# Performance work log

Measured on AMD Instinct MI355X. Metric: run time of the kernel, lower is better.

Reference implementation:

```python
import jax, jax.numpy as jnp
import numpy as np


def setup_inputs() -> dict:
    key = jax.random.key(0)
    ks = jax.random.split(key, 9)
    bs, nf, h, w = 4, 512, 64, 64
    c8 = nf // 8
    sc = 1.0 / np.sqrt(nf)
    return {
        "x": jax.random.normal(ks[0], (bs, nf, h, w), dtype=jnp.float32),
        "Wq": jax.random.normal(ks[1], (c8, nf), dtype=jnp.float32) * sc,
        "bq": jax.random.normal(ks[2], (c8,), dtype=jnp.float32) * 0.01,
        "Wk": jax.random.normal(ks[3], (c8, nf), dtype=jnp.float32) * sc,
        "bk": jax.random.normal(ks[4], (c8,), dtype=jnp.float32) * 0.01,
        "Wv": jax.random.normal(ks[5], (nf, nf), dtype=jnp.float32) * sc,
        "bv": jax.random.normal(ks[6], (nf,), dtype=jnp.float32) * 0.01,
        "alpha": jax.random.normal(ks[7], (1,), dtype=jnp.float32) * 0.1,
    }


def reference(x, Wq, bq, Wk, bk, Wv, bv, alpha):
    bs, nf, h, w = x.shape
    hw = h * w
    xf = x.reshape(bs, nf, hw)  # flatten spatial; 1x1 conv == channel matmul
    q = jnp.einsum('oc,bcn->bon', Wq, xf) + bq[:, None]  # (bs, c8, hw)
    k = jnp.einsum('oc,bcn->bon', Wk, xf) + bk[:, None]  # (bs, c8, hw)
    v = jnp.einsum('oc,bcn->bon', Wv, xf) + bv[:, None]  # (bs, nf, hw)
    # scores[b, i, j] = key_i . query_j ; softmax over j (queries)
    scores = jnp.einsum('bci,bcj->bij', k, q)  # (bs, hw, hw)
    attn = jax.nn.softmax(scores, axis=-1)
    # out[b, c, i] = sum_j v[b, c, j] * attn[b, i, j]
    out = jnp.einsum('bcj,bij->bci', v, attn).reshape(bs, nf, h, w)
    return x + alpha * out
```

## Files before the change

kernel.cpp:

```cpp
#include <hip/hip_runtime.h>

#define BS 4
#define NF 512
#define HW 4096
#define C8 64
#define TI 64
#define JC 64

typedef unsigned short bfu;
typedef __attribute__((ext_vector_type(8))) short bf16x8;
typedef __attribute__((ext_vector_type(4))) float f32x4;

static __device__ __forceinline__ bfu f2bu(float v) {
    union { unsigned int u; float f; } c; c.f = v;
    unsigned int u = c.u;
    u = u + 0x7FFFu + ((u >> 16) & 1u);
    return (bfu)(u >> 16);
}

static __device__ __forceinline__ unsigned int cvt_pk_bf16(float lo, float hi) {
    unsigned int r;
    asm("v_cvt_pk_bf16_f32 %0, %1, %2" : "=v"(r) : "v"(lo), "v"(hi));
    return r;
}

static __device__ __forceinline__ void gload16(const void* g, void* l) {
    __builtin_amdgcn_global_load_lds(
        (const __attribute__((address_space(1))) unsigned int*)g,
        (__attribute__((address_space(3))) unsigned int*)l,
        16, 0, 0);
}

__global__ __launch_bounds__(256) void k0_pre(const float* __restrict__ x, bfu* __restrict__ xt,
                                              const float* __restrict__ Wq, const float* __restrict__ bq,
                                              const float* __restrict__ Wk, const float* __restrict__ bk,
                                              const float* __restrict__ Wv, const float* __restrict__ bv,
                                              bfu* __restrict__ Wb, float* __restrict__ bcat)
{
    __shared__ float T[64][68];
    const int t   = threadIdx.x;
    const int bid = blockIdx.x;

    if (bid >= 2048) {
        const int o = bid - 2048;
        const float* src; float bias;
        if (o < 64)       { src = Wq + (size_t)o * NF;          bias = bq[o]; }
        else if (o < 128) { src = Wk + (size_t)(o - 64) * NF;   bias = bk[o - 64]; }
        else              { src = Wv + (size_t)(o - 128) * NF;  bias = bv[o - 128]; }
        float2 v = *(const float2*)(src + t * 2);
        Wb[(size_t)o * NF + t * 2 + 0] = f2bu(v.x);
        Wb[(size_t)o * NF + t * 2 + 1] = f2bu(v.y);
        if (t == 0) bcat[o] = bias;
        return;
    }

    const int n0 = (bid & 63) * 64;
    const int c0 = ((bid >> 6) & 7) * 64;
    const int b  = bid >> 9;

    #pragma unroll
    for (int u = 0; u < 4; u++) {
        int f4 = u * 256 + t;
        int cc = f4 >> 4;
        int n4 = (f4 & 15) << 2;
        float4 v = *(const float4*)(x + ((size_t)(b * NF + c0 + cc)) * HW + n0 + n4);
        *(float4*)&T[cc][n4 ^ (((cc >> 3) & 3) << 2)] = v;
    }
    __syncthreads();
    #pragma unroll
    for (int u = 0; u < 2; u++) {
        int e8 = u * 256 + t;
        int nn = e8 >> 3;
        int c8 = (e8 & 7) << 3;
        union { int4 i4; bfu h[8]; } pk;
        #pragma unroll
        for (int q = 0; q < 8; q++)
            pk.h[q] = f2bu(T[c8 + q][nn ^ ((((c8 + q) >> 3) & 3) << 2)]);
        *(int4*)(xt + ((size_t)(b * HW + n0 + nn)) * NF + c0 + c8) = pk.i4;
    }
}

__global__ __launch_bounds__(256) void k1_proj(const bfu* __restrict__ Wb, const float* __restrict__ bcat,
                                               const bfu* __restrict__ xt,
                                               bfu* __restrict__ Qb, bfu* __restrict__ Kb, bfu* __restrict__ Vb)
{
    __shared__ bfu As[2][128 * 64];
    __shared__ bfu Bs[2][128 * 64];
    const int t  = threadIdx.x;
    const int o0 = blockIdx.x * 128;
    const int n0 = blockIdx.y * 128;
    const int b  = blockIdx.z;
    const int lane = t & 63, wv = t >> 6;
    const int wm = wv & 1, wn = wv >> 1;
    const int l15 = lane & 15, quad = lane >> 4;
    const int r7  = l15 & 7;
    const int sl0 = (quad ^ r7) * 8;
    const int sl1 = ((quad + 4) ^ r7) * 8;

    const int srow = t >> 3;
    const int scolz = ((t & 7) ^ (srow & 7)) * 8;

    const bfu* gA = Wb + ((size_t)(o0 + srow)) * NF + scolz;
    const bfu* gB = xt + ((size_t)(b * HW + n0 + srow)) * NF + scolz;

    f32x4 acc[4][4];
    #pragma unroll
    for (int m = 0; m < 4; m++)
        #pragma unroll
        for (int n = 0; n < 4; n++) acc[m][n] = (f32x4){0.f, 0.f, 0.f, 0.f};

#define K1_STAGE(buf, c0)                                                       \
    _Pragma("unroll")                                                           \
    for (int p = 0; p < 4; p++) {                                               \
        gload16(gA + (size_t)(p * 32) * NF + (c0), &As[buf][t * 8 + p * 2048]); \
        gload16(gB + (size_t)(p * 32) * NF + (c0), &Bs[buf][t * 8 + p * 2048]); \
    }

#define K1_COMPUTE(pc)                                                                      \
    {                                                                                       \
        bf16x8 Af0[4], Af1[4], Bf0[4], Bf1[4];                                              \
        _Pragma("unroll")                                                                   \
        for (int m = 0; m < 4; m++) {                                                       \
            const bfu* ar = &As[pc][(wm * 64 + m * 16 + l15) * 64];                         \
            Af0[m] = *(const bf16x8*)(ar + sl0);                                            \
            Af1[m] = *(const bf16x8*)(ar + sl1);                                            \
        }                                                                                   \
        _Pragma("unroll")                                                                   \
        for (int n = 0; n < 4; n++) {                                                       \
            const bfu* br = &Bs[pc][(wn * 64 + n * 16 + l15) * 64];                         \
            Bf0[n] = *(const bf16x8*)(br + sl0);                                            \
            Bf1[n] = *(const bf16x8*)(br + sl1);                                            \
        }                                                                                   \
        __builtin_amdgcn_s_setprio(1);                                                      \
        _Pragma("unroll")                                                                   \
        for (int m = 0; m < 4; m++)                                                         \
            _Pragma("unroll")                                                               \
            for (int n = 0; n < 4; n++) {                                                   \
                acc[m][n] = __builtin_amdgcn_mfma_f32_16x16x32_bf16(Af0[m], Bf0[n], acc[m][n], 0, 0, 0); \
                acc[m][n] = __builtin_amdgcn_mfma_f32_16x16x32_bf16(Af1[m], Bf1[n], acc[m][n], 0, 0, 0); \
            }                                                                               \
        __builtin_amdgcn_s_setprio(0);                                                      \
    }

    K1_STAGE(0, 0)
    for (int it = 0; it < 7; it++) {
        const int pc = it & 1;
        K1_STAGE(pc ^ 1, (it + 1) * 64)
        asm volatile("s_waitcnt vmcnt(8)" ::: "memory");
        __builtin_amdgcn_sched_barrier(0);
        __builtin_amdgcn_s_barrier();
        K1_COMPUTE(pc)
        __builtin_amdgcn_sched_barrier(0);
        __builtin_amdgcn_s_barrier();
    }
    asm volatile("s_waitcnt vmcnt(0)" ::: "memory");
    __builtin_amdgcn_sched_barrier(0);
    __builtin_amdgcn_s_barrier();
    K1_COMPUTE(1)
#undef K1_STAGE
#undef K1_COMPUTE

    if (o0 == 0) {
        #pragma unroll
        for (int mt = 0; mt < 4; mt++)
            #pragma unroll
            for (int nt = 0; nt < 4; nt++) {
                int goq = wm * 64 + mt * 16 + quad * 4;
                int n   = n0 + wn * 64 + nt * 16 + l15;
                float v0 = acc[mt][nt][0] + bcat[goq + 0];
                float v1 = acc[mt][nt][1] + bcat[goq + 1];
                float v2 = acc[mt][nt][2] + bcat[goq + 2];
                float v3 = acc[mt][nt][3] + bcat[goq + 3];
                int2 pk;
                pk.x = (int)cvt_pk_bf16(v0, v1);
                pk.y = (int)cvt_pk_bf16(v2, v3);
                if (wm == 0) *(int2*)(Qb + ((size_t)(b * HW + n)) * C8 + goq)      = pk;
                else         *(int2*)(Kb + ((size_t)(b * HW + n)) * C8 + goq - 64) = pk;
            }
    } else {
        #pragma unroll
        for (int mt = 0; mt < 4; mt++)
            #pragma unroll
            for (int nt = 0; nt < 4; nt++)
                #pragma unroll
                for (int r = 0; r < 4; r++) {
                    int go = o0 + wm * 64 + mt * 16 + quad * 4 + r;
                    int n  = n0 + wn * 64 + nt * 16 + l15;
                    float val = acc[mt][nt][r] + bcat[go];
                    Vb[((size_t)(b * NF + (go - 128))) * HW + n] = f2bu(val);
                }
    }
}

__global__ __launch_bounds__(512, 4) void k23_fused(const bfu* __restrict__ Kb, const bfu* __restrict__ Qb,
                                                    const bfu* __restrict__ Vb,
                                                    const float* __restrict__ x, const float* __restrict__ alpha,
                                                    float* __restrict__ out)
{
    __shared__ bfu   Vs[2][256 * 64];
    __shared__ bfu   Ps[64 * 64];
    __shared__ float LSum[8][2][16];
    __shared__ float Scale[TI];

    const int t = threadIdx.x;
    const int lane = t & 63, w = t >> 6;
    const int l15 = lane & 15, quad = lane >> 4;
    const int jq  = w & 3;
    const int iqb = (w >> 2) * 32;

    const int d    = blockIdx.x;
    const int xcd  = d & 7;
    const int b    = xcd >> 1;
    const int cblk = xcd & 1;
    const int i0   = (d >> 3) * TI;

    const bfu* kp0 = Kb + ((size_t)(b * HW + i0 + iqb + l15)) * C8 + quad * 8;
    const bfu* kp1 = kp0 + (size_t)16 * C8;
    const bf16x8 Kf00 = *(const bf16x8*)kp0;
    const bf16x8 Kf01 = *(const bf16x8*)(kp0 + 32);
    const bf16x8 Kf10 = *(const bf16x8*)kp1;
    const bf16x8 Kf11 = *(const bf16x8*)(kp1 + 32);

    const int srow = t >> 3, sslot = t & 7;
    const bfu* gV = Vb + ((size_t)(b * NF + cblk * 256 + srow)) * HW + ((sslot ^ (srow & 7)) * 8);

    const bfu* qbase = Qb + ((size_t)(b * HW + jq * 16 + l15)) * C8 + quad * 8;

    const int r7  = l15 & 7;
    const int sl0 = (quad ^ r7) * 8;
    const int sl1 = ((quad + 4) ^ r7) * 8;
    const int pwz = ((jq * 2 + (quad >> 1)) ^ r7) * 8 + (quad & 1) * 4;

    f32x4 acc[2][4];
    #pragma unroll
    for (int mt = 0; mt < 2; mt++)
        #pragma unroll
        for (int nt = 0; nt < 4; nt++) acc[mt][nt] = (f32x4){0.f, 0.f, 0.f, 0.f};
    float rs0 = 0.f, rs1 = 0.f;
    bf16x8 Aq[2][2];

    Aq[0][0] = *(const bf16x8*)qbase;
    Aq[0][1] = *(const bf16x8*)(qbase + 32);
    #pragma unroll
    for (int p = 0; p < 4; p++)
        gload16(gV + (size_t)(p * 64) * HW, &Vs[0][t * 8 + p * 4096]);
    {
        f32x4 s0 = (f32x4){0.f,0.f,0.f,0.f}, s1 = (f32x4){0.f,0.f,0.f,0.f};
        s0 = __builtin_amdgcn_mfma_f32_16x16x32_bf16(Aq[0][0], Kf00, s0, 0, 0, 0);
        s0 = __builtin_amdgcn_mfma_f32_16x16x32_bf16(Aq[0][1], Kf01, s0, 0, 0, 0);
        s1 = __builtin_amdgcn_mfma_f32_16x16x32_bf16(Aq[0][0], Kf10, s1, 0, 0, 0);
        s1 = __builtin_amdgcn_mfma_f32_16x16x32_bf16(Aq[0][1], Kf11, s1, 0, 0, 0);
        float e0 = __expf(s0[0]), e1 = __expf(s0[1]), e2 = __expf(s0[2]), e3 = __expf(s0[3]);
        float f0 = __expf(s1[0]), f1 = __expf(s1[1]), f2 = __expf(s1[2]), f3 = __expf(s1[3]);
        rs0 += (e0 + e1) + (e2 + e3);
        rs1 += (f0 + f1) + (f2 + f3);
        uint2 pk0, pk1;
        pk0.x = cvt_pk_bf16(e0, e1);  pk0.y = cvt_pk_bf16(e2, e3);
        pk1.x = cvt_pk_bf16(f0, f1);  pk1.y = cvt_pk_bf16(f2, f3);
        *(uint2*)(Ps + (iqb + l15)      * 64 + pwz) = pk0;
        *(uint2*)(Ps + (iqb + 16 + l15) * 64 + pwz) = pk1;
    }

#define K23_ITER(q, pc, pn)                                                                    \
  {                                                                                            \
    const int jn = (((q) + 1) & 63) * JC;                                                      \
                                      \
    {                                                                                          \
        const bfu* qpn = qbase + (size_t)jn * C8;                                              \
        Aq[pn][0] = *(const bf16x8*)qpn;                                                       \
        Aq[pn][1] = *(const bf16x8*)(qpn + 32);                                                \
    }                                                                                          \
    _Pragma("unroll")                                                                          \
    for (int p = 0; p < 4; p++)                                                                \
        gload16(gV + (size_t)(p * 64) * HW + jn, &Vs[pn][t * 8 + p * 4096]);                   \
             \
    asm volatile("s_waitcnt vmcnt(6) lgkmcnt(0)" ::: "memory");                                \
    __builtin_amdgcn_sched_barrier(0);                                                         \
    __builtin_amdgcn_s_barrier();                        \
                    \
    f32x4 s0 = (f32x4){0.f,0.f,0.f,0.f}, s1 = (f32x4){0.f,0.f,0.f,0.f};                        \
    if (jn) {                                                                                  \
        s0 = __builtin_amdgcn_mfma_f32_16x16x32_bf16(Aq[pn][0], Kf00, s0, 0, 0, 0);            \
        s0 = __builtin_amdgcn_mfma_f32_16x16x32_bf16(Aq[pn][1], Kf01, s0, 0, 0, 0);            \
        s1 = __builtin_amdgcn_mfma_f32_16x16x32_bf16(Aq[pn][0], Kf10, s1, 0, 0, 0);            \
        s1 = __builtin_amdgcn_mfma_f32_16x16x32_bf16(Aq[pn][1], Kf11, s1, 0, 0, 0);            \
    }                                                                                          \
                                     \
    {                                                                                          \
        bf16x8 V0[2], V1[2];                                                                   \
        _Pragma("unroll")                                                                      \
        for (int mt = 0; mt < 2; mt++) {                                                       \
            const bfu* vrow = &Vs[pc][(w * 32 + mt * 16 + l15) * 64];                          \
            V0[mt] = *(const bf16x8*)(vrow + sl0);                                             \
            V1[mt] = *(const bf16x8*)(vrow + sl1);                                             \
        }                                                                                      \
        __builtin_amdgcn_s_setprio(1);                                                         \
        _Pragma("unroll")                                                                      \
        for (int nt = 0; nt < 4; nt++) {                                                       \
            const bfu* prow = Ps + (nt * 16 + l15) * 64;                                       \
            bf16x8 Pf0 = *(const bf16x8*)(prow + sl0);                                         \
            bf16x8 Pf1 = *(const bf16x8*)(prow + sl1);                                         \
            _Pragma("unroll")                                                                  \
            for (int mt = 0; mt < 2; mt++) {                                                   \
                acc[mt][nt] = __builtin_amdgcn_mfma_f32_16x16x32_bf16(V0[mt], Pf0, acc[mt][nt], 0, 0, 0); \
                acc[mt][nt] = __builtin_amdgcn_mfma_f32_16x16x32_bf16(V1[mt], Pf1, acc[mt][nt], 0, 0, 0); \
            }                                                                                  \
        }                                                                                      \
        __builtin_amdgcn_s_setprio(0);                                                         \
    }                                                                                          \
    asm volatile("s_waitcnt lgkmcnt(0)" ::: "memory");                                         \
    __builtin_amdgcn_sched_barrier(0);                                                         \
    __builtin_amdgcn_s_barrier();        \
                                 \
    if (jn) {                                                                                  \
        float e0 = __expf(s0[0]), e1 = __expf(s0[1]), e2 = __expf(s0[2]), e3 = __expf(s0[3]);  \
        float f0 = __expf(s1[0]), f1 = __expf(s1[1]), f2 = __expf(s1[2]), f3 = __expf(s1[3]);  \
        rs0 += (e0 + e1) + (e2 + e3);                                                          \
        rs1 += (f0 + f1) + (f2 + f3);                                                          \
        uint2 pk0, pk1;                                                                        \
        pk0.x = cvt_pk_bf16(e0, e1);  pk0.y = cvt_pk_bf16(e2, e3);                             \
        pk1.x = cvt_pk_bf16(f0, f1);  pk1.y = cvt_pk_bf16(f2, f3);                             \
        *(uint2*)(Ps + (iqb + l15)      * 64 + pwz) = pk0;                                     \
        *(uint2*)(Ps + (iqb + 16 + l15) * 64 + pwz) = pk1;                                     \
    }                                                                                          \
  }

    for (int qq = 0; qq < 32; qq++) {
        K23_ITER(2 * qq,     0, 1)
        K23_ITER(2 * qq + 1, 1, 0)
    }
#undef K23_ITER

    float sred0 = rs0, sred1 = rs1;
    sred0 += __shfl_xor(sred0, 16, 64);
    sred0 += __shfl_xor(sred0, 32, 64);
    sred1 += __shfl_xor(sred1, 16, 64);
    sred1 += __shfl_xor(sred1, 32, 64);
    if (quad == 0) { LSum[w][0][l15] = sred0; LSum[w][1][l15] = sred1; }
    __syncthreads();
    if (t < TI) {
        int u = t >> 5, s = (t >> 4) & 1, il = t & 15;
        float L = (LSum[u * 4 + 0][s][il] + LSum[u * 4 + 1][s][il])
                + (LSum[u * 4 + 2][s][il] + LSum[u * 4 + 3][s][il]);
        Scale[t] = alpha[0] / L;
    }
    __syncthreads();

    #pragma unroll
    for (int nt = 0; nt < 4; nt++) {
        float sc = Scale[nt * 16 + l15];
        int i = i0 + nt * 16 + l15;
        #pragma unroll
        for (int mt = 0; mt < 2; mt++)
            #pragma unroll
            for (int r = 0; r < 4; r++) {
                int c = cblk * 256 + w * 32 + mt * 16 + quad * 4 + r;
                size_t idx = ((size_t)(b * NF + c)) * HW + i;
                out[idx] = x[idx] + sc * acc[mt][nt][r];
            }
    }
}

extern "C" void kernel_launch(void* const* d_in, const int* in_sizes, int n_in,
                              void* d_out, int out_size, void* d_ws, size_t ws_size,
                              hipStream_t stream)
{
    const float* x     = (const float*)d_in[0];
    const float* Wq    = (const float*)d_in[1];
    const float* bq    = (const float*)d_in[2];
    const float* Wk    = (const float*)d_in[3];
    const float* bk    = (const float*)d_in[4];
    const float* Wv    = (const float*)d_in[5];
    const float* bv    = (const float*)d_in[6];
    const float* alpha = (const float*)d_in[7];
    float* out = (float*)d_out;

    char* ws = (char*)d_ws;
    bfu*   xt   = (bfu*)(ws);
    bfu*   Wb   = (bfu*)(ws + (16u << 20));
    float* bcat = (float*)(ws + (17u << 20));
    bfu*   Qb   = (bfu*)(ws + (18u << 20));
    bfu*   Kb   = (bfu*)(ws + (20u << 20));
    bfu*   Vb   = (bfu*)(ws + (22u << 20));

    k0_pre<<<dim3(2048 + 640), 256, 0, stream>>>(x, xt, Wq, bq, Wk, bk, Wv, bv, Wb, bcat);
    k1_proj<<<dim3(5, HW / 128, BS), 256, 0, stream>>>(Wb, bcat, xt, Qb, Kb, Vb);
    k23_fused<<<dim3(HW / TI * BS * 2), 512, 0, stream>>>(Kb, Qb, Vb, x, alpha, out);
}
```

Measured before the change: 218.8 us.

## Double-buffer P tile in LDS to drop one barrier per iteration

The softmax probability tile P now has two LDS buffers. Each iteration reads one buffer while writing the next, which removes the second wait-and-barrier in every j-step of the fused attention loop. The V prefetch moves to after the single barrier and writes into the other V buffer, with the wait count changed to match. The row-sum and scale scratch arrays now reuse the P buffer memory. The cost is 8KB more LDS per block and a later start for the V prefetch, which leaves less time to hide it behind the MFMA work.

Result: slower. 228.4 us (+4.4%).

```diff
diff --git a/kernel.cpp b/kernel.cpp
--- a/kernel.cpp
+++ b/kernel.cpp
@@ -197,10 +197,8 @@
                                                     const float* __restrict__ x, const float* __restrict__ alpha,
                                                     float* __restrict__ out)
 {
-    __shared__ bfu   Vs[2][256 * 64];
-    __shared__ bfu   Ps[64 * 64];
-    __shared__ float LSum[8][2][16];
-    __shared__ float Scale[TI];
+    __shared__ bfu Vs[2][256 * 64];
+    __shared__ bfu Psb[2][64 * 64];
 
     const int t = threadIdx.x;
     const int lane = t & 63, w = t >> 6;
@@ -237,19 +235,19 @@
         #pragma unroll
         for (int nt = 0; nt < 4; nt++) acc[mt][nt] = (f32x4){0.f, 0.f, 0.f, 0.f};
     float rs0 = 0.f, rs1 = 0.f;
-    bf16x8 Aq[2][2];
-
-    Aq[0][0] = *(const bf16x8*)qbase;
-    Aq[0][1] = *(const bf16x8*)(qbase + 32);
+    bf16x8 Aq0, Aq1;
+
+    Aq0 = *(const bf16x8*)qbase;
+    Aq1 = *(const bf16x8*)(qbase + 32);
     #pragma unroll
     for (int p = 0; p < 4; p++)
         gload16(gV + (size_t)(p * 64) * HW, &Vs[0][t * 8 + p * 4096]);
     {
         f32x4 s0 = (f32x4){0.f,0.f,0.f,0.f}, s1 = (f32x4){0.f,0.f,0.f,0.f};
-        s0 = __builtin_amdgcn_mfma_f32_16x16x32_bf16(Aq[0][0], Kf00, s0, 0, 0, 0);
-        s0 = __builtin_amdgcn_mfma_f32_16x16x32_bf16(Aq[0][1], Kf01, s0, 0, 0, 0);
-        s1 = __builtin_amdgcn_mfma_f32_16x16x32_bf16(Aq[0][0], Kf10, s1, 0, 0, 0);
-        s1 = __builtin_amdgcn_mfma_f32_16x16x32_bf16(Aq[0][1], Kf11, s1, 0, 0, 0);
+        s0 = __builtin_amdgcn_mfma_f32_16x16x32_bf16(Aq0, Kf00, s0, 0, 0, 0);
+        s0 = __builtin_amdgcn_mfma_f32_16x16x32_bf16(Aq1, Kf01, s0, 0, 0, 0);
+        s1 = __builtin_amdgcn_mfma_f32_16x16x32_bf16(Aq0, Kf10, s1, 0, 0, 0);
+        s1 = __builtin_amdgcn_mfma_f32_16x16x32_bf16(Aq1, Kf11, s1, 0, 0, 0);
         float e0 = __expf(s0[0]), e1 = __expf(s0[1]), e2 = __expf(s0[2]), e3 = __expf(s0[3]);
         float f0 = __expf(s1[0]), f1 = __expf(s1[1]), f2 = __expf(s1[2]), f3 = __expf(s1[3]);
         rs0 += (e0 + e1) + (e2 + e3);
@@ -257,47 +255,50 @@
         uint2 pk0, pk1;
         pk0.x = cvt_pk_bf16(e0, e1);  pk0.y = cvt_pk_bf16(e2, e3);
         pk1.x = cvt_pk_bf16(f0, f1);  pk1.y = cvt_pk_bf16(f2, f3);
-        *(uint2*)(Ps + (iqb + l15)      * 64 + pwz) = pk0;
-        *(uint2*)(Ps + (iqb + 16 + l15) * 64 + pwz) = pk1;
-    }
-
-#define K23_ITER(q, pc, pn)                                                                    \
+        *(uint2*)(&Psb[0][0] + (iqb + l15)      * 64 + pwz) = pk0;
+        *(uint2*)(&Psb[0][0] + (iqb + 16 + l15) * 64 + pwz) = pk1;
+    }
+
+#define K23_ITER(q, pb)                                                                        \
   {                                                                                            \
-    const int jn = (((q) + 1) & 63) * JC;                                                      \
-                                      \
+    const int jn = (((q) + 1) & 63) * JC;      \
+             \
     {                                                                                          \
         const bfu* qpn = qbase + (size_t)jn * C8;                                              \
-        Aq[pn][0] = *(const bf16x8*)qpn;                                                       \
-        Aq[pn][1] = *(const bf16x8*)(qpn + 32);                                                \
-    }                                                                                          \
-    _Pragma("unroll")                                                                          \
-    for (int p = 0; p < 4; p++)                                                                \
-        gload16(gV + (size_t)(p * 64) * HW + jn, &Vs[pn][t * 8 + p * 4096]);                   \
-             \
-    asm volatile("s_waitcnt vmcnt(6) lgkmcnt(0)" ::: "memory");                                \
+        Aq0 = *(const bf16x8*)qpn;                                                             \
+        Aq1 = *(const bf16x8*)(qpn + 32);                                                      \
+    }                                                                                          \
+                         \
+    asm volatile("s_waitcnt vmcnt(2) lgkmcnt(0)" ::: "memory");                                \
     __builtin_amdgcn_sched_barrier(0);                                                         \
-    __builtin_amdgcn_s_barrier();                        \
-                    \
+    __builtin_amdgcn_s_barrier();    \
+                \
+    if (jn) {                                                                                  \
+        _Pragma("unroll")                                                                      \
+        for (int p = 0; p < 4; p++)                                                            \
+            gload16(gV + (size_t)(p * 64) * HW + jn, &Vs[pb ^ 1][t * 8 + p * 4096]);           \
+    }                                                                                          \
+                      \
     f32x4 s0 = (f32x4){0.f,0.f,0.f,0.f}, s1 = (f32x4){0.f,0.f,0.f,0.f};                        \
     if (jn) {                                                                                  \
-        s0 = __builtin_amdgcn_mfma_f32_16x16x32_bf16(Aq[pn][0], Kf00, s0, 0, 0, 0);            \
-        s0 = __builtin_amdgcn_mfma_f32_16x16x32_bf16(Aq[pn][1], Kf01, s0, 0, 0, 0);            \
-        s1 = __builtin_amdgcn_mfma_f32_16x16x32_bf16(Aq[pn][0], Kf10, s1, 0, 0, 0);            \
-        s1 = __builtin_amdgcn_mfma_f32_16x16x32_bf16(Aq[pn][1], Kf11, s1, 0, 0, 0);            \
-    }                                                                                          \
-                                     \
+        s0 = __builtin_amdgcn_mfma_f32_16x16x32_bf16(Aq0, Kf00, s0, 0, 0, 0);                  \
+        s0 = __builtin_amdgcn_mfma_f32_16x16x32_bf16(Aq1, Kf01, s0, 0, 0, 0);                  \
+        s1 = __builtin_amdgcn_mfma_f32_16x16x32_bf16(Aq0, Kf10, s1, 0, 0, 0);                  \
+        s1 = __builtin_amdgcn_mfma_f32_16x16x32_bf16(Aq1, Kf11, s1, 0, 0, 0);                  \
+    }                                                                                          \
+                                                    \
     {                                                                                          \
         bf16x8 V0[2], V1[2];                                                                   \
         _Pragma("unroll")                                                                      \
         for (int mt = 0; mt < 2; mt++) {                                                       \
-            const bfu* vrow = &Vs[pc][(w * 32 + mt * 16 + l15) * 64];                          \
+            const bfu* vrow = &Vs[pb][(w * 32 + mt * 16 + l15) * 64];                          \
             V0[mt] = *(const bf16x8*)(vrow + sl0);                                             \
             V1[mt] = *(const bf16x8*)(vrow + sl1);                                             \
         }                                                                                      \
         __builtin_amdgcn_s_setprio(1);                                                         \
         _Pragma("unroll")                                                                      \
         for (int nt = 0; nt < 4; nt++) {                                                       \
-            const bfu* prow = Ps + (nt * 16 + l15) * 64;                                       \
+            const bfu* prow = &Psb[pb][0] + (nt * 16 + l15) * 64;                              \
             bf16x8 Pf0 = *(const bf16x8*)(prow + sl0);                                         \
             bf16x8 Pf1 = *(const bf16x8*)(prow + sl1);                                         \
             _Pragma("unroll")                                                                  \
@@ -308,10 +309,7 @@
         }                                                                                      \
         __builtin_amdgcn_s_setprio(0);                                                         \
     }                                                                                          \
-    asm volatile("s_waitcnt lgkmcnt(0)" ::: "memory");                                         \
-    __builtin_amdgcn_sched_barrier(0);                                                         \
-    __builtin_amdgcn_s_barrier();        \
-                                 \
+                \
     if (jn) {                                                                                  \
         float e0 = __expf(s0[0]), e1 = __expf(s0[1]), e2 = __expf(s0[2]), e3 = __expf(s0[3]);  \
         float f0 = __expf(s1[0]), f1 = __expf(s1[1]), f2 = __expf(s1[2]), f3 = __expf(s1[3]);  \
@@ -320,28 +318,30 @@
         uint2 pk0, pk1;                                                                        \
         pk0.x = cvt_pk_bf16(e0, e1);  pk0.y = cvt_pk_bf16(e2, e3);                             \
         pk1.x = cvt_pk_bf16(f0, f1);  pk1.y = cvt_pk_bf16(f2, f3);                             \
-        *(uint2*)(Ps + (iqb + l15)      * 64 + pwz) = pk0;                                     \
-        *(uint2*)(Ps + (iqb + 16 + l15) * 64 + pwz) = pk1;                                     \
+        *(uint2*)(&Psb[pb ^ 1][0] + (iqb + l15)      * 64 + pwz) = pk0;                        \
+        *(uint2*)(&Psb[pb ^ 1][0] + (iqb + 16 + l15) * 64 + pwz) = pk1;                        \
     }                                                                                          \
   }
 
     for (int qq = 0; qq < 32; qq++) {
-        K23_ITER(2 * qq,     0, 1)
-        K23_ITER(2 * qq + 1, 1, 0)
+        K23_ITER(2 * qq,     0)
+        K23_ITER(2 * qq + 1, 1)
     }
 #undef K23_ITER
 
+    float* LSum  = (float*)&Psb[0][0];
+    float* Scale = (float*)&Psb[0][2048];
     float sred0 = rs0, sred1 = rs1;
     sred0 += __shfl_xor(sred0, 16, 64);
     sred0 += __shfl_xor(sred0, 32, 64);
     sred1 += __shfl_xor(sred1, 16, 64);
     sred1 += __shfl_xor(sred1, 32, 64);
-    if (quad == 0) { LSum[w][0][l15] = sred0; LSum[w][1][l15] = sred1; }
+    if (quad == 0) { LSum[(w * 2 + 0) * 16 + l15] = sred0; LSum[(w * 2 + 1) * 16 + l15] = sred1; }
     __syncthreads();
     if (t < TI) {
         int u = t >> 5, s = (t >> 4) & 1, il = t & 15;
-        float L = (LSum[u * 4 + 0][s][il] + LSum[u * 4 + 1][s][il])
-                + (LSum[u * 4 + 2][s][il] + LSum[u * 4 + 3][s][il]);
+        float L = (LSum[((u * 4 + 0) * 2 + s) * 16 + il] + LSum[((u * 4 + 1) * 2 + s) * 16 + il])
+                + (LSum[((u * 4 + 2) * 2 + s) * 16 + il] + LSum[((u * 4 + 3) * 2 + s) * 16 + il]);
         Scale[t] = alpha[0] / L;
     }
     __syncthreads();
```
